# Optimization experiments

Measured on AMD Instinct MI355X. Metric: run time of the kernel, lower is better.

The kernel has to match this reference:

```python
import jax, jax.numpy as jnp
import numpy as np

N = 50000; E = 800000
IN = 128; H = 4; D = 32; OH = H * D; AIN = 2 * IN
SCALE = float(1.0 / np.sqrt(IN))

def _ln(x, g, b):
    m = jnp.mean(x, -1, keepdims=True)
    v = jnp.mean((x - m) ** 2, -1, keepdims=True)
    return (x - m) * jax.lax.rsqrt(v + 1e-5) * g + b

def setup_inputs():
    keys = iter(jax.random.split(jax.random.key(0), 24))
    nrm = lambda shape, s=1.0: jax.random.normal(next(keys), shape, dtype=jnp.float32) * s
    inp = {}
    inp['x0'] = nrm((N, IN)); inp['x1'] = nrm((N, IN)); inp['x99'] = nrm((N, AIN))
    inp['feat0'] = jax.random.uniform(next(keys), (E, 2), dtype=jnp.float32)
    inp['feat1'] = jax.random.uniform(next(keys), (E, 2), dtype=jnp.float32)
    for nm, shape in [('Wq', (IN, OH)), ('Wk', (IN, OH)), ('Wv', (IN, OH)), ('Wo', (OH, OH)), ('Wffn', (IN, OH)), ('Waq', (AIN, OH)), ('Wak', (AIN, OH)), ('Wav', (AIN, OH)), ('Wao', (OH, OH)), ('Waffn', (AIN, OH))]:
        inp[nm] = nrm(shape, 0.05)
    for nm in ['bq', 'bk', 'bv', 'bo', 'bffn', 'baq', 'bak', 'bav', 'bao', 'baffn', 'ln_b', 'aln_b']:
        inp[nm] = jnp.zeros((OH,), jnp.float32)
    inp['ln_g'] = jnp.ones((OH,), jnp.float32); inp['aln_g'] = jnp.ones((OH,), jnp.float32)
    for nm in ['src0', 'dst0', 'src1', 'dst1']:
        inp[nm] = jax.random.randint(next(keys), (E,), 0, N, dtype=jnp.int32)
    return inp

def _forward(x0, x1, x99, feat0, feat1, Wq, bq, Wk, bk, Wv, bv, Wo, bo, Wffn, bffn, ln_g, ln_b, Waq, baq, Wak, bak, Wav, bav, Wao, bao, Waffn, baffn, aln_g, aln_b, src0, dst0, src1, dst1):
    proj = lambda x, W, b: (x @ W + b).reshape(x.shape[0], H, D)
    xs = (x0, x1)
    edges = ((src0, dst0, feat0), (src1, dst1, feat1))
    q = [proj(x, Wq, bq) for x in xs]   # per-v_id linears are shared
    k = [proj(x, Wk, bk) for x in xs]
    v = [proj(x, Wv, bv) for x in xs]
    q99 = proj(x99, Waq, baq); k99 = proj(x99, Wak, bak); v99 = proj(x99, Wav, bav)
    aggr_outs = []
    for i, (src, dst, feat) in enumerate(edges):  # loop over the 2 edge types (structural)
        f = feat[:, None, 0:1]  # [E,1,1] 'connect' edge weight
        s = jnp.sum(k[i][src] * q[i][dst], -1, keepdims=True) * f   # [E,H,1]
        s99 = jnp.sum(k99[src] * q99[dst], -1, keepdims=True) * f
        s = jnp.exp(jnp.clip(s * SCALE, -5.0, 5.0))
        s99 = jnp.exp(jnp.clip(s99 * SCALE, -5.0, 5.0))
        wv = jax.ops.segment_sum(v[i][src] * s, dst, num_segments=N)    # [N,H,D]
        z = jax.ops.segment_sum(s, dst, num_segments=N)                 # [N,H,1]
        wv99 = jax.ops.segment_sum(v99[src] * s99, dst, num_segments=N)
        z99 = jax.ops.segment_sum(s99, dst, num_segments=N)
        # per-v_id branch (h_dict in original; computed but not returned by the module)
        o = (wv / (z + 1.0)).reshape(N, OH) @ Wo + bo
        h = xs[i] @ Wffn + bffn + o
        h = h + _ln(h, ln_g, ln_b)
        # aggregated (node 99) branch -> returned as aggr_h_dict[v_id]
        ao = (wv99 / (z99 + 1.0)).reshape(N, OH) @ Wao + bao
        ah = x99 @ Waffn + baffn + ao
        ah = ah + _ln(ah, aln_g, aln_b)
        aggr_outs.append(ah)
    return tuple(aggr_outs)

def reference(x0, x1, x99, feat0, feat1, Wq, bq, Wk, bk, Wv, bv, Wo, bo, Wffn, bffn, ln_g, ln_b, Waq, baq, Wak, bak, Wav, bav, Wao, bao, Waffn, baffn, aln_g, aln_b, src0, dst0, src1, dst1):
    return _forward(x0, x1, x99, feat0, feat1, Wq, bq, Wk, bk, Wv, bv, Wo, bo, Wffn, bffn, ln_g, ln_b, Waq, baq, Wak, bak, Wav, bav, Wao, bao, Waffn, baffn, aln_g, aln_b, src0, dst0, src1, dst1)
```

## Files before the change

### kernel.cpp

```cpp
#include <hip/hip_runtime.h>
#include <math.h>

#define NN 50000
#define EE 800000
#define AIN 256
#define OH 128

#define NTOT  (2 * NN)
#define NB    391
#define CAP   5120
#define MT    391
#define RPX   49

typedef __attribute__((ext_vector_type(8))) short bf16x8;
typedef __attribute__((ext_vector_type(4))) float f32x4;
typedef __attribute__((ext_vector_type(2))) float f32x2;

static __device__ __forceinline__ unsigned short f2bf(float f) {
    union { float f; unsigned int u; } v; v.f = f;
    return (unsigned short)((v.u + 0x7FFFu + ((v.u >> 16) & 1u)) >> 16);
}
static __device__ __forceinline__ float bflo(unsigned int u) { return __uint_as_float(u << 16); }
static __device__ __forceinline__ float bfhi(unsigned int u) { return __uint_as_float(u & 0xFFFF0000u); }

__global__ __launch_bounds__(256) void cvt_x_k(const float* __restrict__ x, unsigned short* __restrict__ xb)
{
    const int i = blockIdx.x * 256 + threadIdx.x;
    if (i >= NN * AIN / 4) return;
    const float4 v = ((const float4*)x)[i];
    ushort4 o;
    o.x = f2bf(v.x); o.y = f2bf(v.y); o.z = f2bf(v.z); o.w = f2bf(v.w);
    ((ushort4*)xb)[i] = o;
}

__global__ __launch_bounds__(256) void cvt_w_k(
    const float* __restrict__ Wq, const float* __restrict__ Wk,
    const float* __restrict__ Wv, const float* __restrict__ Wf,
    const float* __restrict__ Wo, unsigned short* __restrict__ Wt,
    unsigned short* __restrict__ Waot)
{
    const int n = blockIdx.x;
    const int k = threadIdx.x;
    if (n < 512) {
        const float* W = (n < 128) ? Wq : (n < 256) ? Wk : (n < 384) ? Wv : Wf;
        Wt[(size_t)n * 256 + k] = f2bf(W[(size_t)k * OH + (n & 127)]);
    } else {
        if (k < 128) Waot[(size_t)(n - 512) * 128 + k] = f2bf(Wo[(size_t)k * OH + (n - 512)]);
    }
}

__global__ __launch_bounds__(256) void qkvf_mfma_k(
    const unsigned short* __restrict__ xb,
    const unsigned short* __restrict__ Wt,
    const float* __restrict__ bq, const float* __restrict__ bk,
    const float* __restrict__ bv, const float* __restrict__ bf,
    unsigned short* __restrict__ qb, unsigned char* __restrict__ kv8,
    unsigned short* __restrict__ ffnb, int M)
{
    const int nblk = blockIdx.x;
    const int xcd  = nblk & 7;
    const int slot = nblk >> 3;
    const int rowt = xcd * RPX + (slot >> 2);
    const int y    = slot & 3;
    if (rowt >= MT) return;

    __shared__ unsigned short As[128][40];
    __shared__ unsigned short Bs[128][40];
    const int tid  = threadIdx.x;
    const int lane = tid & 63;
    const int wave = tid >> 6;
    const int wr = wave >> 1, wc = wave & 1;
    const int quad = lane >> 4, m16 = lane & 15;
    const int row0 = rowt * 128;
    const int col0 = y * 128;

    f32x4 acc[4][4];
    #pragma unroll
    for (int i = 0; i < 4; ++i)
        #pragma unroll
        for (int j = 0; j < 4; ++j) acc[i][j] = 0.f;

    const int lr  = tid >> 1;
    const int lkh = (tid & 1) * 16;

    for (int kt = 0; kt < 256; kt += 32) {
        uint4 a0 = {0,0,0,0}, a1 = {0,0,0,0};
        const int grow = row0 + lr;
        if (grow < M) {
            const uint4* p = (const uint4*)(xb + (size_t)grow * 256 + kt + lkh);
            a0 = p[0]; a1 = p[1];
        }
        *(uint4*)&As[lr][lkh]     = a0;
        *(uint4*)&As[lr][lkh + 8] = a1;
        const uint4* wp = (const uint4*)(Wt + (size_t)(col0 + lr) * 256 + kt + lkh);
        *(uint4*)&Bs[lr][lkh]     = wp[0];
        *(uint4*)&Bs[lr][lkh + 8] = wp[1];
        __syncthreads();
        bf16x8 af[4], bfr[4];
        #pragma unroll
        for (int t = 0; t < 4; ++t) af[t]  = *(const bf16x8*)&As[wr * 64 + t * 16 + m16][quad * 8];
        #pragma unroll
        for (int t = 0; t < 4; ++t) bfr[t] = *(const bf16x8*)&Bs[wc * 64 + t * 16 + m16][quad * 8];
        #pragma unroll
        for (int i = 0; i < 4; ++i)
            #pragma unroll
            for (int j = 0; j < 4; ++j)
                acc[i][j] = __builtin_amdgcn_mfma_f32_16x16x32_bf16(af[i], bfr[j], acc[i][j], 0, 0, 0);
        __syncthreads();
    }

    const float* bias = (y == 0) ? bq : (y == 1) ? bk : (y == 2) ? bv : bf;

    if (y == 1 || y == 2) {
        const int ocol = (y == 2) ? 128 : 0;
        #pragma unroll
        for (int i = 0; i < 4; ++i)
            #pragma unroll
            for (int j = 0; j < 4; ++j) {
                const int col = wc * 64 + j * 16 + m16;
                const float b = bias[col];
                #pragma unroll
                for (int r = 0; r < 4; ++r) {
                    const int row = row0 + wr * 64 + i * 16 + quad * 4 + r;
                    if (row < M) {
                        const unsigned int pk =
                            (unsigned int)__builtin_amdgcn_cvt_pk_fp8_f32(acc[i][j][r] + b, 0.f, 0, 0);
                        kv8[(size_t)row * 256 + ocol + col] = (unsigned char)(pk & 0xFF);
                    }
                }
            }
    } else {
        unsigned short* obase = (y == 3) ? ffnb : qb;
        #pragma unroll
        for (int i = 0; i < 4; ++i)
            #pragma unroll
            for (int j = 0; j < 4; ++j) {
                const int col = wc * 64 + j * 16 + m16;
                const float b = bias[col];
                #pragma unroll
                for (int r = 0; r < 4; ++r) {
                    const int row = row0 + wr * 64 + i * 16 + quad * 4 + r;
                    if (row < M) obase[(size_t)row * 128 + col] = f2bf(acc[i][j][r] + b);
                }
            }
    }
}

__global__ __launch_bounds__(256) void binpass_k(
    const int* __restrict__ dst0, const int* __restrict__ dst1,
    const int* __restrict__ src0, const int* __restrict__ src1,
    const float* __restrict__ feat0, const float* __restrict__ feat1,
    int* __restrict__ cursor, uint2* __restrict__ stage)
{
    __shared__ int hcnt[NB], blkbase[NB], lcur[NB];
    const int tid = threadIdx.x;
    const long base = (long)blockIdx.x * 8192;

    for (int i = tid; i < NB; i += 256) { hcnt[i] = 0; lcur[i] = 0; }
    __syncthreads();

    for (int i = tid; i < 8192; i += 256) {
        const long e = base + i;
        if (e < 2L * EE) {
            const int nid = (e < EE) ? dst0[e] : NN + dst1[e - EE];
            atomicAdd(&hcnt[nid >> 8], 1);
        }
    }
    __syncthreads();
    for (int i = tid; i < NB; i += 256)
        if (hcnt[i]) blkbase[i] = atomicAdd(&cursor[i], hcnt[i]);
    __syncthreads();

    for (int i = tid; i < 8192; i += 256) {
        const long e = base + i;
        if (e < 2L * EE) {
            const bool a = (e < EE);
            const int ee = a ? (int)e : (int)(e - EE);
            const int nid = a ? dst0[ee] : NN + dst1[ee];
            const int s = a ? src0[ee] : src1[ee];
            const float f = a ? feat0[(size_t)ee * 2] : feat1[(size_t)ee * 2];
            const int bk = nid >> 8;
            const int r = atomicAdd(&lcur[bk], 1);
            uint2 rec;
            rec.x = __float_as_uint(f);
            rec.y = ((unsigned int)s << 8) | (unsigned int)(nid & 255);
            stage[(size_t)bk * CAP + blkbase[bk] + r] = rec;
        }
    }
}

__global__ __launch_bounds__(512) void bscan_k(const int* __restrict__ cursor, int* __restrict__ bbase)
{
    __shared__ int part[512];
    const int t = threadIdx.x;
    const int v = (t < NB) ? cursor[t] : 0;
    part[t] = v;
    __syncthreads();
    for (int st = 1; st < 512; st <<= 1) {
        int u = (t >= st) ? part[t - st] : 0;
        __syncthreads();
        part[t] += u;
        __syncthreads();
    }
    if (t < NB) bbase[t] = part[t] - v;
}

__global__ __launch_bounds__(256) void sortpass_k(
    const uint2* __restrict__ stage, const int* __restrict__ cursor,
    const int* __restrict__ bbase, unsigned int* __restrict__ erec,
    int* __restrict__ off, int* __restrict__ deg)
{
    __shared__ uint2 srec[CAP];
    __shared__ int h[256], eb[256], cur[256];
    const int b = blockIdx.x;
    const int t = threadIdx.x;
    const int cntb = min(cursor[b], CAP);
    const int obase = bbase[b];
    const uint2* sb = stage + (size_t)b * CAP;

    h[t] = 0; cur[t] = 0;
    for (int i = t; i < cntb; i += 256) srec[i] = sb[i];
    __syncthreads();
    for (int i = t; i < cntb; i += 256) atomicAdd(&h[(int)(srec[i].y & 255u)], 1);
    __syncthreads();
    eb[t] = h[t];
    __syncthreads();
    for (int st = 1; st < 256; st <<= 1) {
        int u = (t >= st) ? eb[t - st] : 0;
        __syncthreads();
        eb[t] += u;
        __syncthreads();
    }
    const int incl = eb[t];
    __syncthreads();
    eb[t] = incl - h[t];
    __syncthreads();

    const int nid = b * 256 + t;
    if (nid < NTOT) {
        off[nid] = obase + eb[t];
        deg[nid] = h[t];
    }

    for (int i = t; i < cntb; i += 256) {
        const uint2 r = srec[i];
        const int loc = (int)(r.y & 255u);
        const int rk = atomicAdd(&cur[loc], 1);
        const unsigned int f15 = __float2uint_rn(__uint_as_float(r.x) * 32767.f);
        erec[obase + eb[loc] + rk] = ((r.y >> 8) << 15) | f15;
    }
}

__global__ __launch_bounds__(256) void aggregate_k(
    const unsigned short* __restrict__ qb, const unsigned char* __restrict__ kv8,
    const unsigned int* __restrict__ erec,
    const int* __restrict__ off, const int* __restrict__ deg,
    unsigned short* __restrict__ att)
{
    const int nid = blockIdx.x * 4 + (threadIdx.x >> 6);
    if (nid >= NTOT) return;
    const int n = (nid >= NN) ? nid - NN : nid;
    const int lane = threadIdx.x & 63;
    const int g   = lane >> 4;
    const int d16 = lane & 15;
    const int start = off[nid];
    const int count = deg[nid];

    const uint4 qu = *(const uint4*)(qb + (size_t)n * 128 + d16 * 8);
    f32x2 qd0, qd1, qd2, qd3;
    qd0[0] = bflo(qu.x); qd0[1] = bfhi(qu.x);
    qd1[0] = bflo(qu.y); qd1[1] = bfhi(qu.y);
    qd2[0] = bflo(qu.z); qd2[1] = bfhi(qu.z);
    qd3[0] = bflo(qu.w); qd3[1] = bfhi(qu.w);

    f32x2 av0 = 0.f, av1 = 0.f, av2 = 0.f, av3 = 0.f;
    float zp = 0.f;
    const float SCALE = 0.088388347648318447f;
    const float FDEQ  = 1.0f / 32767.0f;
    const unsigned char* kvl = kv8 + d16 * 8;

    for (int base = 0; base < count; base += 64) {
        const int m = min(64, count - base);
        const unsigned int ue = erec[start + base + min(lane, m - 1)];
        unsigned int cu = (unsigned int)__shfl((int)ue, g);
        const unsigned char* rp = kvl + (size_t)(cu >> 15) * 256;
        uint2 kc = *(const uint2*)rp;
        uint2 vc = *(const uint2*)(rp + 128);
        for (int j0 = 0; j0 < m; j0 += 4) {
            const uint2 kk = kc;
            const uint2 vv = vc;
            const float f = (float)(cu & 32767u) * FDEQ;
            const int jn = j0 + 4;
            if (jn < m) {
                cu = (unsigned int)__shfl((int)ue, jn + g);
                const unsigned char* rn = kvl + (size_t)(cu >> 15) * 256;
                kc = *(const uint2*)rn;
                vc = *(const uint2*)(rn + 128);
            }
            const f32x2 k0 = __builtin_amdgcn_cvt_pk_f32_fp8((int)kk.x, false);
            const f32x2 k1 = __builtin_amdgcn_cvt_pk_f32_fp8((int)kk.x, true);
            const f32x2 k2 = __builtin_amdgcn_cvt_pk_f32_fp8((int)kk.y, false);
            const f32x2 k3 = __builtin_amdgcn_cvt_pk_f32_fp8((int)kk.y, true);
            f32x2 p2 = k0 * qd0;
            p2 += k1 * qd1;
            p2 += k2 * qd2;
            p2 += k3 * qd3;
            float p = p2[0] + p2[1];
            p += __shfl_xor(p, 1);
            p += __shfl_xor(p, 2);
            float sc = __expf(fminf(5.f, fmaxf(-5.f, p * f * SCALE)));
            sc = (j0 + g < m) ? sc : 0.f;
            zp += sc;
            const f32x2 v0 = __builtin_amdgcn_cvt_pk_f32_fp8((int)vv.x, false);
            const f32x2 v1 = __builtin_amdgcn_cvt_pk_f32_fp8((int)vv.x, true);
            const f32x2 v2 = __builtin_amdgcn_cvt_pk_f32_fp8((int)vv.y, false);
            const f32x2 v3 = __builtin_amdgcn_cvt_pk_f32_fp8((int)vv.y, true);
            f32x2 sc2; sc2[0] = sc; sc2[1] = sc;
            av0 += v0 * sc2;
            av1 += v1 * sc2;
            av2 += v2 * sc2;
            av3 += v3 * sc2;
        }
    }

    float z = zp;
    z += __shfl_xor(z, 16);
    z += __shfl_xor(z, 32);
    av0[0] += __shfl_xor(av0[0], 16); av0[0] += __shfl_xor(av0[0], 32);
    av0[1] += __shfl_xor(av0[1], 16); av0[1] += __shfl_xor(av0[1], 32);
    av1[0] += __shfl_xor(av1[0], 16); av1[0] += __shfl_xor(av1[0], 32);
    av1[1] += __shfl_xor(av1[1], 16); av1[1] += __shfl_xor(av1[1], 32);
    av2[0] += __shfl_xor(av2[0], 16); av2[0] += __shfl_xor(av2[0], 32);
    av2[1] += __shfl_xor(av2[1], 16); av2[1] += __shfl_xor(av2[1], 32);
    av3[0] += __shfl_xor(av3[0], 16); av3[0] += __shfl_xor(av3[0], 32);
    av3[1] += __shfl_xor(av3[1], 16); av3[1] += __shfl_xor(av3[1], 32);

    const float inv = 1.f / (z + 1.f);
    const f32x2 e01 = (g & 1) ? av1 : av0;
    const f32x2 e23 = (g & 1) ? av3 : av2;
    const f32x2 e   = (g & 2) ? e23 : e01;
    const float ax = e[0] * inv;
    const float ay = e[1] * inv;
    const unsigned int o = ((unsigned int)f2bf(ay) << 16) | (unsigned int)f2bf(ax);
    *(unsigned int*)(att + (size_t)nid * 128 + d16 * 8 + g * 2) = o;
}

__global__ __launch_bounds__(256) void attn_out_mfma_k(
    const unsigned short* __restrict__ attAll, const unsigned short* __restrict__ Wt,
    const float* __restrict__ bo, const unsigned short* __restrict__ ffnb,
    const float* __restrict__ g, const float* __restrict__ bln,
    float* __restrict__ Yall, int M)
{
    const int nblk = blockIdx.x;
    const int xcd  = nblk & 7;
    const int slot = nblk >> 3;
    const int rowt = xcd * RPX + (slot >> 1);
    const int set  = slot & 1;
    if (rowt >= MT) return;

    __shared__ unsigned short As[128][40];
    __shared__ unsigned short Bs[128][40];
    __shared__ float rsum[2][128], rsq[2][128];
    __shared__ float meanar[128], invar[128];

    const unsigned short* att = attAll + (size_t)set * NN * 128;
    float* Y = Yall + (size_t)set * NN * 128;

    const int tid  = threadIdx.x;
    const int lane = tid & 63;
    const int wave = tid >> 6;
    const int wr = wave >> 1, wc = wave & 1;
    const int quad = lane >> 4, m16 = lane & 15;
    const int row0 = rowt * 128;

    f32x4 acc[4][4];
    #pragma unroll
    for (int i = 0; i < 4; ++i)
        #pragma unroll
        for (int j = 0; j < 4; ++j) acc[i][j] = 0.f;

    const int lr  = tid >> 1;
    const int lkh = (tid & 1) * 16;

    for (int kt = 0; kt < 128; kt += 32) {
        uint4 a0 = {0,0,0,0}, a1 = {0,0,0,0};
        const int grow = row0 + lr;
        if (grow < M) {
            const uint4* p = (const uint4*)(att + (size_t)grow * 128 + kt + lkh);
            a0 = p[0]; a1 = p[1];
        }
        *(uint4*)&As[lr][lkh]     = a0;
        *(uint4*)&As[lr][lkh + 8] = a1;
        const uint4* wp = (const uint4*)(Wt + (size_t)lr * 128 + kt + lkh);
        *(uint4*)&Bs[lr][lkh]     = wp[0];
        *(uint4*)&Bs[lr][lkh + 8] = wp[1];
        __syncthreads();
        bf16x8 af[4], bfr[4];
        #pragma unroll
        for (int t = 0; t < 4; ++t) af[t]  = *(const bf16x8*)&As[wr * 64 + t * 16 + m16][quad * 8];
        #pragma unroll
        for (int t = 0; t < 4; ++t) bfr[t] = *(const bf16x8*)&Bs[wc * 64 + t * 16 + m16][quad * 8];
        #pragma unroll
        for (int i = 0; i < 4; ++i)
            #pragma unroll
            for (int j = 0; j < 4; ++j)
                acc[i][j] = __builtin_amdgcn_mfma_f32_16x16x32_bf16(af[i], bfr[j], acc[i][j], 0, 0, 0);
        __syncthreads();
    }

    #pragma unroll
    for (int i = 0; i < 4; ++i) {
        #pragma unroll
        for (int r = 0; r < 4; ++r) {
            const int rl = wr * 64 + i * 16 + quad * 4 + r;
            const int grow = row0 + rl;
            float s = 0.f, q = 0.f;
            #pragma unroll
            for (int j = 0; j < 4; ++j) {
                const int col = wc * 64 + j * 16 + m16;
                float v = acc[i][j][r] + bo[col];
                if (grow < M) v += bflo(ffnb[(size_t)grow * 128 + col]);
                acc[i][j][r] = v;
                s += v; q += v * v;
            }
            #pragma unroll
            for (int mm = 1; mm <= 8; mm <<= 1) {
                s += __shfl_xor(s, mm, 16);
                q += __shfl_xor(q, mm, 16);
            }
            if (m16 == 0) { rsum[wc][rl] = s; rsq[wc][rl] = q; }
        }
    }
    __syncthreads();
    if (tid < 128) {
        const float s = rsum[0][tid] + rsum[1][tid];
        const float q = rsq[0][tid] + rsq[1][tid];
        const float mean = s * (1.f / 128.f);
        const float var  = q * (1.f / 128.f) - mean * mean;
        meanar[tid] = mean;
        invar[tid]  = rsqrtf(fmaxf(var, 0.f) + 1e-5f);
    }
    __syncthreads();

    #pragma unroll
    for (int i = 0; i < 4; ++i) {
        #pragma unroll
        for (int j = 0; j < 4; ++j) {
            const int col = wc * 64 + j * 16 + m16;
            const float gv = g[col], lv = bln[col];
            #pragma unroll
            for (int r = 0; r < 4; ++r) {
                const int rl = wr * 64 + i * 16 + quad * 4 + r;
                const int grow = row0 + rl;
                if (grow < M) {
                    const float v = acc[i][j][r];
                    Y[(size_t)grow * 128 + col] = v + (v - meanar[rl]) * invar[rl] * gv + lv;
                }
            }
        }
    }
}

extern "C" void kernel_launch(void* const* d_in, const int* in_sizes, int n_in,
                              void* d_out, int out_size, void* d_ws, size_t ws_size,
                              hipStream_t stream) {
    const float* x99   = (const float*)d_in[2];
    const float* feat0 = (const float*)d_in[3];
    const float* feat1 = (const float*)d_in[4];
    const float* Waq   = (const float*)d_in[10];
    const float* Wak   = (const float*)d_in[11];
    const float* Wav   = (const float*)d_in[12];
    const float* Wao   = (const float*)d_in[13];
    const float* Waffn = (const float*)d_in[14];
    const float* baq   = (const float*)d_in[20];
    const float* bak   = (const float*)d_in[21];
    const float* bav   = (const float*)d_in[22];
    const float* bao   = (const float*)d_in[23];
    const float* baffn = (const float*)d_in[24];
    const float* aln_b = (const float*)d_in[26];
    const float* aln_g = (const float*)d_in[28];
    const int* src0 = (const int*)d_in[29];
    const int* dst0 = (const int*)d_in[30];
    const int* src1 = (const int*)d_in[31];
    const int* dst1 = (const int*)d_in[32];

    unsigned short* xb   = (unsigned short*)d_ws;
    unsigned short* qb   = xb + (size_t)NN * 256;
    unsigned char*  kv8  = (unsigned char*)(qb + (size_t)NN * 128);
    unsigned short* ffnb = (unsigned short*)(kv8 + (size_t)NN * 256);
    unsigned short* att  = ffnb + (size_t)NN * 128;
    unsigned short* Wt   = att  + (size_t)NTOT * 128;
    unsigned short* Waot = Wt   + (size_t)512 * 256;
    int* cursor = (int*)(Waot + 128 * 128);
    int* bbase  = cursor + NB;
    int* off    = bbase + NB;
    int* deg    = off + NTOT;

    float* out = (float*)d_out;
    uint2* stage = (uint2*)d_out;
    unsigned int* erec = (unsigned int*)(stage + (size_t)NB * CAP);

    cvt_x_k<<<(NN * AIN / 4 + 255) / 256, 256, 0, stream>>>(x99, xb);
    cvt_w_k<<<640, 256, 0, stream>>>(Waq, Wak, Wav, Waffn, Wao, Wt, Waot);

    qkvf_mfma_k<<<8 * RPX * 4, 256, 0, stream>>>(xb, Wt, baq, bak, bav, baffn, qb, kv8, ffnb, NN);

    hipMemsetAsync(cursor, 0, NB * sizeof(int), stream);
    binpass_k<<<(2 * EE + 8191) / 8192, 256, 0, stream>>>(
        dst0, dst1, src0, src1, feat0, feat1, cursor, stage);
    bscan_k<<<1, 512, 0, stream>>>(cursor, bbase);
    sortpass_k<<<NB, 256, 0, stream>>>(stage, cursor, bbase, erec, off, deg);

    aggregate_k<<<(NTOT + 3) / 4, 256, 0, stream>>>(qb, kv8, erec, off, deg, att);
    attn_out_mfma_k<<<8 * RPX * 2, 256, 0, stream>>>(att, Waot, bao, ffnb, aln_g, aln_b, out, NN);
}
```

Baseline: 431.8 us.

## Fuse preprocessing kernels, drop scan kernel, interleave K/V fp8 for single loads

Result: slower. 507.6 us (+17.6%).

```diff
diff --git a/kernel.cpp b/kernel.cpp
--- a/kernel.cpp
+++ b/kernel.cpp
@@ -11,6 +11,12 @@
 #define CAP   5120
 #define MT    391
 #define RPX   49
+
+#define F1_CVTX  12500
+#define F1_CVTW  640
+#define F1_BIN   196
+#define F2_QKVF  (8 * RPX * 4)
+#define F2_SMEM  29696
 
 typedef __attribute__((ext_vector_type(8))) short bf16x8;
 typedef __attribute__((ext_vector_type(4))) float f32x4;
@@ -23,138 +29,44 @@
 static __device__ __forceinline__ float bflo(unsigned int u) { return __uint_as_float(u << 16); }
 static __device__ __forceinline__ float bfhi(unsigned int u) { return __uint_as_float(u & 0xFFFF0000u); }
 
-__global__ __launch_bounds__(256) void cvt_x_k(const float* __restrict__ x, unsigned short* __restrict__ xb)
-{
-    const int i = blockIdx.x * 256 + threadIdx.x;
-    if (i >= NN * AIN / 4) return;
-    const float4 v = ((const float4*)x)[i];
-    ushort4 o;
-    o.x = f2bf(v.x); o.y = f2bf(v.y); o.z = f2bf(v.z); o.w = f2bf(v.w);
-    ((ushort4*)xb)[i] = o;
-}
-
-__global__ __launch_bounds__(256) void cvt_w_k(
+__global__ __launch_bounds__(256) void fuse1_k(
+    const float* __restrict__ x99, unsigned short* __restrict__ xb,
     const float* __restrict__ Wq, const float* __restrict__ Wk,
     const float* __restrict__ Wv, const float* __restrict__ Wf,
     const float* __restrict__ Wo, unsigned short* __restrict__ Wt,
-    unsigned short* __restrict__ Waot)
-{
-    const int n = blockIdx.x;
-    const int k = threadIdx.x;
-    if (n < 512) {
-        const float* W = (n < 128) ? Wq : (n < 256) ? Wk : (n < 384) ? Wv : Wf;
-        Wt[(size_t)n * 256 + k] = f2bf(W[(size_t)k * OH + (n & 127)]);
-    } else {
-        if (k < 128) Waot[(size_t)(n - 512) * 128 + k] = f2bf(Wo[(size_t)k * OH + (n - 512)]);
-    }
-}
-
-__global__ __launch_bounds__(256) void qkvf_mfma_k(
-    const unsigned short* __restrict__ xb,
-    const unsigned short* __restrict__ Wt,
-    const float* __restrict__ bq, const float* __restrict__ bk,
-    const float* __restrict__ bv, const float* __restrict__ bf,
-    unsigned short* __restrict__ qb, unsigned char* __restrict__ kv8,
-    unsigned short* __restrict__ ffnb, int M)
-{
-    const int nblk = blockIdx.x;
-    const int xcd  = nblk & 7;
-    const int slot = nblk >> 3;
-    const int rowt = xcd * RPX + (slot >> 2);
-    const int y    = slot & 3;
-    if (rowt >= MT) return;
-
-    __shared__ unsigned short As[128][40];
-    __shared__ unsigned short Bs[128][40];
-    const int tid  = threadIdx.x;
-    const int lane = tid & 63;
-    const int wave = tid >> 6;
-    const int wr = wave >> 1, wc = wave & 1;
-    const int quad = lane >> 4, m16 = lane & 15;
-    const int row0 = rowt * 128;
-    const int col0 = y * 128;
-
-    f32x4 acc[4][4];
-    #pragma unroll
-    for (int i = 0; i < 4; ++i)
-        #pragma unroll
-        for (int j = 0; j < 4; ++j) acc[i][j] = 0.f;
-
-    const int lr  = tid >> 1;
-    const int lkh = (tid & 1) * 16;
-
-    for (int kt = 0; kt < 256; kt += 32) {
-        uint4 a0 = {0,0,0,0}, a1 = {0,0,0,0};
-        const int grow = row0 + lr;
-        if (grow < M) {
-            const uint4* p = (const uint4*)(xb + (size_t)grow * 256 + kt + lkh);
-            a0 = p[0]; a1 = p[1];
-        }
-        *(uint4*)&As[lr][lkh]     = a0;
-        *(uint4*)&As[lr][lkh + 8] = a1;
-        const uint4* wp = (const uint4*)(Wt + (size_t)(col0 + lr) * 256 + kt + lkh);
-        *(uint4*)&Bs[lr][lkh]     = wp[0];
-        *(uint4*)&Bs[lr][lkh + 8] = wp[1];
-        __syncthreads();
-        bf16x8 af[4], bfr[4];
-        #pragma unroll
-        for (int t = 0; t < 4; ++t) af[t]  = *(const bf16x8*)&As[wr * 64 + t * 16 + m16][quad * 8];
-        #pragma unroll
-        for (int t = 0; t < 4; ++t) bfr[t] = *(const bf16x8*)&Bs[wc * 64 + t * 16 + m16][quad * 8];
-        #pragma unroll
-        for (int i = 0; i < 4; ++i)
-            #pragma unroll
-            for (int j = 0; j < 4; ++j)
-                acc[i][j] = __builtin_amdgcn_mfma_f32_16x16x32_bf16(af[i], bfr[j], acc[i][j], 0, 0, 0);
-        __syncthreads();
-    }
-
-    const float* bias = (y == 0) ? bq : (y == 1) ? bk : (y == 2) ? bv : bf;
-
-    if (y == 1 || y == 2) {
-        const int ocol = (y == 2) ? 128 : 0;
-        #pragma unroll
-        for (int i = 0; i < 4; ++i)
-            #pragma unroll
-            for (int j = 0; j < 4; ++j) {
-                const int col = wc * 64 + j * 16 + m16;
-                const float b = bias[col];
-                #pragma unroll
-                for (int r = 0; r < 4; ++r) {
-                    const int row = row0 + wr * 64 + i * 16 + quad * 4 + r;
-                    if (row < M) {
-                        const unsigned int pk =
-                            (unsigned int)__builtin_amdgcn_cvt_pk_fp8_f32(acc[i][j][r] + b, 0.f, 0, 0);
-                        kv8[(size_t)row * 256 + ocol + col] = (unsigned char)(pk & 0xFF);
-                    }
-                }
-            }
-    } else {
-        unsigned short* obase = (y == 3) ? ffnb : qb;
-        #pragma unroll
-        for (int i = 0; i < 4; ++i)
-            #pragma unroll
-            for (int j = 0; j < 4; ++j) {
-                const int col = wc * 64 + j * 16 + m16;
-                const float b = bias[col];
-                #pragma unroll
-                for (int r = 0; r < 4; ++r) {
-                    const int row = row0 + wr * 64 + i * 16 + quad * 4 + r;
-                    if (row < M) obase[(size_t)row * 128 + col] = f2bf(acc[i][j][r] + b);
-                }
-            }
-    }
-}
-
-__global__ __launch_bounds__(256) void binpass_k(
+    unsigned short* __restrict__ Waot,
     const int* __restrict__ dst0, const int* __restrict__ dst1,
     const int* __restrict__ src0, const int* __restrict__ src1,
     const float* __restrict__ feat0, const float* __restrict__ feat1,
-    int* __restrict__ cursor, uint2* __restrict__ stage)
+    int* __restrict__ cursor, unsigned int* __restrict__ stage_rec,
+    unsigned char* __restrict__ stage_loc)
 {
     __shared__ int hcnt[NB], blkbase[NB], lcur[NB];
+    const int b = blockIdx.x;
     const int tid = threadIdx.x;
-    const long base = (long)blockIdx.x * 8192;
+
+    if (b < F1_CVTX) {
+        const int i = b * 256 + tid;
+        const float4 v = ((const float4*)x99)[i];
+        ushort4 o;
+        o.x = f2bf(v.x); o.y = f2bf(v.y); o.z = f2bf(v.z); o.w = f2bf(v.w);
+        ((ushort4*)xb)[i] = o;
+        return;
+    }
+    if (b < F1_CVTX + F1_CVTW) {
+        const int n = b - F1_CVTX;
+        const int k = tid;
+        if (n < 512) {
+            const float* W = (n < 128) ? Wq : (n < 256) ? Wk : (n < 384) ? Wv : Wf;
+            Wt[(size_t)n * 256 + k] = f2bf(W[(size_t)k * OH + (n & 127)]);
+        } else {
+            if (k < 128) Waot[(size_t)(n - 512) * 128 + k] = f2bf(Wo[(size_t)k * OH + (n - 512)]);
+        }
+        return;
+    }
+
+    const int bb = b - (F1_CVTX + F1_CVTW);
+    const long base = (long)bb * 8192;
 
     for (int i = tid; i < NB; i += 256) { hcnt[i] = 0; lcur[i] = 0; }
     __syncthreads();
@@ -181,47 +93,148 @@
             const float f = a ? feat0[(size_t)ee * 2] : feat1[(size_t)ee * 2];
             const int bk = nid >> 8;
             const int r = atomicAdd(&lcur[bk], 1);
-            uint2 rec;
-            rec.x = __float_as_uint(f);
-            rec.y = ((unsigned int)s << 8) | (unsigned int)(nid & 255);
-            stage[(size_t)bk * CAP + blkbase[bk] + r] = rec;
+            const size_t pos = (size_t)bk * CAP + blkbase[bk] + r;
+            stage_rec[pos] = ((unsigned int)s << 15) | __float2uint_rn(f * 32767.f);
+            stage_loc[pos] = (unsigned char)(nid & 255);
         }
     }
 }
 
-__global__ __launch_bounds__(512) void bscan_k(const int* __restrict__ cursor, int* __restrict__ bbase)
-{
-    __shared__ int part[512];
-    const int t = threadIdx.x;
-    const int v = (t < NB) ? cursor[t] : 0;
-    part[t] = v;
-    __syncthreads();
-    for (int st = 1; st < 512; st <<= 1) {
-        int u = (t >= st) ? part[t - st] : 0;
-        __syncthreads();
-        part[t] += u;
-        __syncthreads();
-    }
-    if (t < NB) bbase[t] = part[t] - v;
-}
-
-__global__ __launch_bounds__(256) void sortpass_k(
-    const uint2* __restrict__ stage, const int* __restrict__ cursor,
-    const int* __restrict__ bbase, unsigned int* __restrict__ erec,
+__global__ __launch_bounds__(256) void fuse2_k(
+    const unsigned short* __restrict__ xb,
+    const unsigned short* __restrict__ Wt,
+    const float* __restrict__ bq, const float* __restrict__ bk,
+    const float* __restrict__ bv, const float* __restrict__ bf,
+    unsigned short* __restrict__ qb, unsigned char* __restrict__ kv8,
+    unsigned short* __restrict__ ffnb, int M,
+    const unsigned int* __restrict__ stage_rec,
+    const unsigned char* __restrict__ stage_loc,
+    const int* __restrict__ cursor, unsigned int* __restrict__ erec,
     int* __restrict__ off, int* __restrict__ deg)
 {
-    __shared__ uint2 srec[CAP];
-    __shared__ int h[256], eb[256], cur[256];
+    __shared__ __align__(16) unsigned char smem[F2_SMEM];
     const int b = blockIdx.x;
-    const int t = threadIdx.x;
-    const int cntb = min(cursor[b], CAP);
-    const int obase = bbase[b];
-    const uint2* sb = stage + (size_t)b * CAP;
+    const int tid = threadIdx.x;
+
+    if (b < F2_QKVF) {
+        const int xcd  = b & 7;
+        const int slot = b >> 3;
+        const int rowt = xcd * RPX + (slot >> 2);
+        const int y    = slot & 3;
+        if (rowt >= MT) return;
+
+        unsigned short (*As)[40] = (unsigned short (*)[40])smem;
+        unsigned short (*Bs)[40] = (unsigned short (*)[40])(smem + 10240);
+
+        const int lane = tid & 63;
+        const int wave = tid >> 6;
+        const int wr = wave >> 1, wc = wave & 1;
+        const int quad = lane >> 4, m16 = lane & 15;
+        const int row0 = rowt * 128;
+        const int col0 = y * 128;
+
+        f32x4 acc[4][4];
+        #pragma unroll
+        for (int i = 0; i < 4; ++i)
+            #pragma unroll
+            for (int j = 0; j < 4; ++j) acc[i][j] = 0.f;
+
+        const int lr  = tid >> 1;
+        const int lkh = (tid & 1) * 16;
+
+        for (int kt = 0; kt < 256; kt += 32) {
+            uint4 a0 = {0,0,0,0}, a1 = {0,0,0,0};
+            const int grow = row0 + lr;
+            if (grow < M) {
+                const uint4* p = (const uint4*)(xb + (size_t)grow * 256 + kt + lkh);
+                a0 = p[0]; a1 = p[1];
+            }
+            *(uint4*)&As[lr][lkh]     = a0;
+            *(uint4*)&As[lr][lkh + 8] = a1;
+            const uint4* wp = (const uint4*)(Wt + (size_t)(col0 + lr) * 256 + kt + lkh);
+            *(uint4*)&Bs[lr][lkh]     = wp[0];
+            *(uint4*)&Bs[lr][lkh + 8] = wp[1];
+            __syncthreads();
+            bf16x8 af[4], bfr[4];
+            #pragma unroll
+            for (int t = 0; t < 4; ++t) af[t]  = *(const bf16x8*)&As[wr * 64 + t * 16 + m16][quad * 8];
+            #pragma unroll
+            for (int t = 0; t < 4; ++t) bfr[t] = *(const bf16x8*)&Bs[wc * 64 + t * 16 + m16][quad * 8];
+            #pragma unroll
+            for (int i = 0; i < 4; ++i)
+                #pragma unroll
+                for (int j = 0; j < 4; ++j)
+                    acc[i][j] = __builtin_amdgcn_mfma_f32_16x16x32_bf16(af[i], bfr[j], acc[i][j], 0, 0, 0);
+            __syncthreads();
+        }
+
+        const float* bias = (y == 0) ? bq : (y == 1) ? bk : (y == 2) ? bv : bf;
+
+        if (y == 1 || y == 2) {
+            const int ocol8 = (y == 2) ? 8 : 0;
+            #pragma unroll
+            for (int i = 0; i < 4; ++i)
+                #pragma unroll
+                for (int j = 0; j < 4; ++j) {
+                    const int col = wc * 64 + j * 16 + m16;
+                    const float bcol = bias[col];
+                    const int bpos = ((col >> 3) << 4) + (col & 7) + ocol8;
+                    #pragma unroll
+                    for (int r = 0; r < 4; ++r) {
+                        const int row = row0 + wr * 64 + i * 16 + quad * 4 + r;
+                        if (row < M) {
+                            const unsigned int pk =
+                                (unsigned int)__builtin_amdgcn_cvt_pk_fp8_f32(acc[i][j][r] + bcol, 0.f, 0, 0);
+                            kv8[(size_t)row * 256 + bpos] = (unsigned char)(pk & 0xFF);
+                        }
+                    }
+                }
+        } else {
+            unsigned short* obase = (y == 3) ? ffnb : qb;
+            #pragma unroll
+            for (int i = 0; i < 4; ++i)
+                #pragma unroll
+                for (int j = 0; j < 4; ++j) {
+                    const int col = wc * 64 + j * 16 + m16;
+                    const float bcol = bias[col];
+                    #pragma unroll
+                    for (int r = 0; r < 4; ++r) {
+                        const int row = row0 + wr * 64 + i * 16 + quad * 4 + r;
+                        if (row < M) obase[(size_t)row * 128 + col] = f2bf(acc[i][j][r] + bcol);
+                    }
+                }
+        }
+        return;
+    }
+
+    const int b2 = b - F2_QKVF;
+    unsigned int*  srec = (unsigned int*)smem;
+    unsigned char* sloc = smem + 20480;
+    int* h   = (int*)(smem + 25600);
+    int* eb  = (int*)(smem + 26624);
+    int* cur = (int*)(smem + 27648);
+    int* red = (int*)(smem + 28672);
+
+    const int t = tid;
+    const int cntb = min(cursor[b2], CAP);
 
     h[t] = 0; cur[t] = 0;
-    for (int i = t; i < cntb; i += 256) srec[i] = sb[i];
-    __syncthreads();
-    for (int i = t; i < cntb; i += 256) atomicAdd(&h[(int)(srec[i].y & 255u)], 1);
+    int pre = 0;
+    for (int i = t; i < b2; i += 256) pre += cursor[i];
+    red[t] = pre;
+    __syncthreads();
+    for (int s = 128; s > 0; s >>= 1) {
+        if (t < s) red[t] += red[t + s];
+        __syncthreads();
+    }
+    const int obase = red[0];
+
+    for (int i = t; i < cntb; i += 256) {
+        srec[i] = stage_rec[(size_t)b2 * CAP + i];
+        sloc[i] = stage_loc[(size_t)b2 * CAP + i];
+    }
+    __syncthreads();
+    for (int i = t; i < cntb; i += 256) atomicAdd(&h[(int)sloc[i]], 1);
     __syncthreads();
     eb[t] = h[t];
     __syncthreads();
@@ -236,18 +249,16 @@
     eb[t] = incl - h[t];
     __syncthreads();
 
-    const int nid = b * 256 + t;
+    const int nid = b2 * 256 + t;
     if (nid < NTOT) {
         off[nid] = obase + eb[t];
         deg[nid] = h[t];
     }
 
     for (int i = t; i < cntb; i += 256) {
-        const uint2 r = srec[i];
-        const int loc = (int)(r.y & 255u);
+        const int loc = (int)sloc[i];
         const int rk = atomicAdd(&cur[loc], 1);
-        const unsigned int f15 = __float2uint_rn(__uint_as_float(r.x) * 32767.f);
-        erec[obase + eb[loc] + rk] = ((r.y >> 8) << 15) | f15;
+        erec[obase + eb[loc] + rk] = srec[i];
     }
 }
 
@@ -275,32 +286,33 @@
 
     f32x2 av0 = 0.f, av1 = 0.f, av2 = 0.f, av3 = 0.f;
     float zp = 0.f;
-    const float SCALE = 0.088388347648318447f;
-    const float FDEQ  = 1.0f / 32767.0f;
-    const unsigned char* kvl = kv8 + d16 * 8;
+    const float FSC = 0.088388347648318447f / 32767.0f;
+    const unsigned char* kvl = kv8 + d16 * 16;
 
     for (int base = 0; base < count; base += 64) {
         const int m = min(64, count - base);
         const unsigned int ue = erec[start + base + min(lane, m - 1)];
-        unsigned int cu = (unsigned int)__shfl((int)ue, g);
-        const unsigned char* rp = kvl + (size_t)(cu >> 15) * 256;
-        uint2 kc = *(const uint2*)rp;
-        uint2 vc = *(const uint2*)(rp + 128);
+        unsigned int cuA = (unsigned int)__shfl((int)ue, g);
+        uint4 ldA = *(const uint4*)(kvl + (size_t)(cuA >> 15) * 256);
+        unsigned int cuB = cuA;
+        uint4 ldB = ldA;
+        if (4 < m) {
+            cuB = (unsigned int)__shfl((int)ue, 4 + g);
+            ldB = *(const uint4*)(kvl + (size_t)(cuB >> 15) * 256);
+        }
         for (int j0 = 0; j0 < m; j0 += 4) {
-            const uint2 kk = kc;
-            const uint2 vv = vc;
-            const float f = (float)(cu & 32767u) * FDEQ;
-            const int jn = j0 + 4;
-            if (jn < m) {
-                cu = (unsigned int)__shfl((int)ue, jn + g);
-                const unsigned char* rn = kvl + (size_t)(cu >> 15) * 256;
-                kc = *(const uint2*)rn;
-                vc = *(const uint2*)(rn + 128);
+            const uint4 kv = ldA;
+            const float fs = (float)(cuA & 32767u) * FSC;
+            cuA = cuB; ldA = ldB;
+            const int j2 = j0 + 8;
+            if (j2 < m) {
+                cuB = (unsigned int)__shfl((int)ue, j2 + g);
+                ldB = *(const uint4*)(kvl + (size_t)(cuB >> 15) * 256);
             }
-            const f32x2 k0 = __builtin_amdgcn_cvt_pk_f32_fp8((int)kk.x, false);
-            const f32x2 k1 = __builtin_amdgcn_cvt_pk_f32_fp8((int)kk.x, true);
-            const f32x2 k2 = __builtin_amdgcn_cvt_pk_f32_fp8((int)kk.y, false);
-            const f32x2 k3 = __builtin_amdgcn_cvt_pk_f32_fp8((int)kk.y, true);
+            const f32x2 k0 = __builtin_amdgcn_cvt_pk_f32_fp8((int)kv.x, false);
+            const f32x2 k1 = __builtin_amdgcn_cvt_pk_f32_fp8((int)kv.x, true);
+            const f32x2 k2 = __builtin_amdgcn_cvt_pk_f32_fp8((int)kv.y, false);
+            const f32x2 k3 = __builtin_amdgcn_cvt_pk_f32_fp8((int)kv.y, true);
             f32x2 p2 = k0 * qd0;
             p2 += k1 * qd1;
             p2 += k2 * qd2;
@@ -308,13 +320,13 @@
             float p = p2[0] + p2[1];
             p += __shfl_xor(p, 1);
             p += __shfl_xor(p, 2);
-            float sc = __expf(fminf(5.f, fmaxf(-5.f, p * f * SCALE)));
+            float sc = __expf(fminf(5.f, fmaxf(-5.f, p * fs)));
             sc = (j0 + g < m) ? sc : 0.f;
             zp += sc;
-            const f32x2 v0 = __builtin_amdgcn_cvt_pk_f32_fp8((int)vv.x, false);
-            const f32x2 v1 = __builtin_amdgcn_cvt_pk_f32_fp8((int)vv.x, true);
-            const f32x2 v2 = __builtin_amdgcn_cvt_pk_f32_fp8((int)vv.y, false);
-            const f32x2 v3 = __builtin_amdgcn_cvt_pk_f32_fp8((int)vv.y, true);
+            const f32x2 v0 = __builtin_amdgcn_cvt_pk_f32_fp8((int)kv.z, false);
+            const f32x2 v1 = __builtin_amdgcn_cvt_pk_f32_fp8((int)kv.z, true);
+            const f32x2 v2 = __builtin_amdgcn_cvt_pk_f32_fp8((int)kv.w, false);
+            const f32x2 v3 = __builtin_amdgcn_cvt_pk_f32_fp8((int)kv.w, true);
             f32x2 sc2; sc2[0] = sc; sc2[1] = sc;
             av0 += v0 * sc2;
             av1 += v1 * sc2;
@@ -492,24 +504,23 @@
     unsigned short* Wt   = att  + (size_t)NTOT * 128;
     unsigned short* Waot = Wt   + (size_t)512 * 256;
     int* cursor = (int*)(Waot + 128 * 128);
-    int* bbase  = cursor + NB;
-    int* off    = bbase + NB;
+    int* off    = cursor + NB;
     int* deg    = off + NTOT;
 
     float* out = (float*)d_out;
-    uint2* stage = (uint2*)d_out;
-    unsigned int* erec = (unsigned int*)(stage + (size_t)NB * CAP);
-
-    cvt_x_k<<<(NN * AIN / 4 + 255) / 256, 256, 0, stream>>>(x99, xb);
-    cvt_w_k<<<640, 256, 0, stream>>>(Waq, Wak, Wav, Waffn, Wao, Wt, Waot);
-
-    qkvf_mfma_k<<<8 * RPX * 4, 256, 0, stream>>>(xb, Wt, baq, bak, bav, baffn, qb, kv8, ffnb, NN);
+    unsigned int*  stage_rec = (unsigned int*)d_out;
+    unsigned char* stage_loc = (unsigned char*)(stage_rec + (size_t)NB * CAP);
+    unsigned int*  erec = (unsigned int*)(stage_loc + (size_t)NB * CAP);
 
     hipMemsetAsync(cursor, 0, NB * sizeof(int), stream);
-    binpass_k<<<(2 * EE + 8191) / 8192, 256, 0, stream>>>(
-        dst0, dst1, src0, src1, feat0, feat1, cursor, stage);
-    bscan_k<<<1, 512, 0, stream>>>(cursor, bbase);
-    sortpass_k<<<NB, 256, 0, stream>>>(stage, cursor, bbase, erec, off, deg);
+
+    fuse1_k<<<F1_CVTX + F1_CVTW + F1_BIN, 256, 0, stream>>>(
+        x99, xb, Waq, Wak, Wav, Waffn, Wao, Wt, Waot,
+        dst0, dst1, src0, src1, feat0, feat1, cursor, stage_rec, stage_loc);
+
+    fuse2_k<<<F2_QKVF + NB, 256, 0, stream>>>(
+        xb, Wt, baq, bak, bav, baffn, qb, kv8, ffnb, NN,
+        stage_rec, stage_loc, cursor, erec, off, deg);
 
     aggregate_k<<<(NTOT + 3) / 4, 256, 0, stream>>>(qb, kv8, erec, off, deg, att);
     attn_out_mfma_k<<<8 * RPX * 2, 256, 0, stream>>>(att, Waot, bao, ffnb, aln_g, aln_b, out, NN);
```
